# Optimization experiments

Measured on AMD Instinct MI355X. Metric: run time of the kernel, lower is better.

The kernel has to match this reference:

```python
import jax, jax.numpy as jnp
import numpy as np

GC = 128      # mem_dim
HEADS = 4     # gc / att_head_dim
HD = 32       # att_head_dim


def _dwconv(x, w, b, pad):
    # depthwise conv, NCHW, weight OIHW with I=1, groups=GC
    y = jax.lax.conv_general_dilated(
        x, w, window_strides=(1, 1),
        padding=((pad[0], pad[0]), (pad[1], pad[1])),
        feature_group_count=GC,
        dimension_numbers=('NCHW', 'OIHW', 'NCHW'))
    return y + b[None, :, None, None]


def setup_inputs() -> dict:
    key = jax.random.key(0)
    ks = jax.random.split(key, 5)
    x = jax.random.normal(ks[0], (32, 512, 56, 56), dtype=jnp.float32)
    w_dw1 = jax.random.normal(ks[1], (GC, 1, 3, 3), dtype=jnp.float32) * 0.1
    b_dw1 = jnp.zeros((GC,), jnp.float32)
    w_dw2 = jax.random.normal(ks[2], (GC, 1, 7, 7), dtype=jnp.float32) * 0.05
    b_dw2 = jnp.zeros((GC,), jnp.float32)
    w_qk = jax.random.normal(ks[3], (2 * GC, GC, 1, 1), dtype=jnp.float32) * (1.0 / np.sqrt(GC))
    b_qk = jnp.zeros((2 * GC,), jnp.float32)
    return {"x": x, "w_dw1": w_dw1, "b_dw1": b_dw1, "w_dw2": w_dw2,
            "b_dw2": b_dw2, "w_qk": w_qk, "b_qk": b_qk}


def reference(x, w_dw1, b_dw1, w_dw2, b_dw2, w_qk, b_qk):
    B, C, H, W = x.shape
    HW = H * W
    # grasp_memory + asymmetric_decouple (split along channels)
    m0 = C - 3 * GC
    mem = x[:, :m0]
    feat_att = x[:, m0:m0 + GC]
    feat_conv1 = x[:, m0 + GC:m0 + 2 * GC]
    feat_conv2 = x[:, m0 + 2 * GC:]
    feat_conv1 = _dwconv(feat_conv1, w_dw1, b_dw1, (1, 1))
    feat_conv2 = _dwconv(feat_conv2, w_dw2, b_dw2, (3, 3))
    # 1x1 conv qk -> [B, 2*GC, H, W]
    qk = jnp.einsum('bchw,oc->bohw', feat_att, w_qk[:, :, 0, 0]) + b_qk[None, :, None, None]
    qk = qk.reshape(B, 2 * GC, HW)
    q = qk[:, :GC].reshape(B, HEADS, HD, HW).transpose(0, 1, 3, 2)   # [B,h,HW,d]
    k = qk[:, GC:].reshape(B, HEADS, HD, HW).transpose(0, 1, 3, 2)
    v = feat_att.reshape(B, HEADS, HD, HW).transpose(0, 1, 3, 2)
    q = jax.nn.elu(q) + 1.0
    k = jax.nn.elu(k) + 1.0
    kmean = k.mean(axis=2, keepdims=True)                            # [B,h,1,d]
    z = 1.0 / (jnp.einsum('bhnd,bhmd->bhnm', q, kmean) + 1e-6)       # [B,h,HW,1]
    kv = jnp.einsum('bhnd,bhne->bhde', k, v) / HW                    # [B,h,d,d]
    att = jnp.einsum('bhnd,bhde->bhne', q, kv) * z                   # [B,h,HW,d]
    feat_att_out = att.transpose(0, 1, 3, 2).reshape(B, GC, H, W)
    feats = jnp.concatenate([feat_att_out, feat_conv1, feat_conv2], axis=1)
    return (mem, feats)
```

## Files before the change

kernel.cpp:

```cpp
#include <hip/hip_runtime.h>
#include <hip/hip_bf16.h>

#define Bn   32
#define Cn   512
#define GCn  128
#define HWn  3136
#define M0   128

#define Q_ELEMS  (Bn*GCn*HWn)
#define KV_ELEMS (Bn*4*32*32)
#define KS_ELEMS (Bn*4*32)

typedef __attribute__((ext_vector_type(8))) short bf16x8;
typedef __attribute__((ext_vector_type(4))) float f32x4;

__device__ __forceinline__ float bf2f(unsigned short u) {
    union { unsigned int i; float f; } v; v.i = ((unsigned int)u) << 16; return v.f;
}
__device__ __forceinline__ unsigned short f2bf(float f) {
    union { __hip_bfloat16 h; unsigned short u; } v; v.h = __float2bfloat16(f); return v.u;
}
__device__ __forceinline__ float act_elu1(float v) {
    return v > 0.0f ? v + 1.0f : __expf(v);
}

__global__ __launch_bounds__(256) void k_pre(
    const float* __restrict__ w_qk, unsigned short* __restrict__ wfrag,
    float* __restrict__ kvz) {
    const int t = threadIdx.x;
    if (blockIdx.x < 128) {
        int idx = blockIdx.x * 256 + t;
        int j  = idx & 7;
        int l  = (idx >> 3) & 63;
        int ks = (idx >> 9) & 3;
        int mt = idx >> 11;
        int o = mt * 16 + (l & 15);
        int c = ks * 32 + (l >> 4) * 8 + j;
        wfrag[idx] = f2bf(w_qk[o * 128 + c]);
    } else {
        int i = (blockIdx.x - 128) * 256 + t;
        kvz[i] = 0.0f;
    }
}

__global__ __launch_bounds__(256) void k_main(
    const float* __restrict__ x, const unsigned short* __restrict__ wfrag,
    const float* __restrict__ b_qk,
    unsigned short* __restrict__ q_ws, float* __restrict__ kv_g,
    float* __restrict__ ks_g) {

    __shared__ unsigned short Xn[64 * 144];
    __shared__ unsigned short Klds[128 * 72];
    unsigned short* Qlds = Xn;

    const int t  = threadIdx.x;
    const int n0 = blockIdx.x * 64;
    const int b  = blockIdx.y;
    const float* xa = x + ((long long)(b * Cn + M0)) * HWn;

    {
        const int c0 = t >> 1, half = t & 1;
        const float* src = xa + (long long)c0 * HWn + n0 + half * 32;
        #pragma unroll
        for (int p = 0; p < 8; ++p) {
            float4 v = *(const float4*)(src + p * 4);
            const int n = half * 32 + p * 4;
            Xn[(n + 0) * 144 + c0] = f2bf(v.x);
            Xn[(n + 1) * 144 + c0] = f2bf(v.y);
            Xn[(n + 2) * 144 + c0] = f2bf(v.z);
            Xn[(n + 3) * 144 + c0] = f2bf(v.w);
        }
    }
    __syncthreads();

    const int w = t >> 6, l = t & 63, nn = l & 15, q = l >> 4;
    f32x4 acc[4][4] = {};

    #pragma unroll
    for (int ks = 0; ks < 4; ++ks) {
        bf16x8 bq[4];
        #pragma unroll
        for (int in = 0; in < 4; ++in)
            bq[in] = *(const bf16x8*)(Xn + (in * 16 + nn) * 144 + ks * 32 + q * 8);
        #pragma unroll
        for (int im = 0; im < 4; ++im) {
            const int mt = 4 * w + im;
            bf16x8 aq = *(const bf16x8*)(wfrag + ((mt * 4 + ks) * 64 + l) * 8);
            #pragma unroll
            for (int in = 0; in < 4; ++in)
                acc[im][in] = __builtin_amdgcn_mfma_f32_16x16x32_bf16(aq, bq[in], acc[im][in], 0, 0, 0);
        }
    }

    if (w >= 2) {
        #pragma unroll
        for (int im = 0; im < 4; ++im) {
            const int obase = w * 64 + im * 16 + q * 4;
            float4 bias4 = *(const float4*)(b_qk + obase);
            const int krow = obase - 128;
            #pragma unroll
            for (int r = 0; r < 4; ++r) {
                const float bias = ((const float*)&bias4)[r];
                #pragma unroll
                for (int in = 0; in < 4; ++in)
                    Klds[(krow + r) * 72 + in * 16 + nn] = f2bf(act_elu1(acc[im][in][r] + bias));
            }
        }
    }
    __syncthreads();

    if (w < 2) {
        #pragma unroll
        for (int im = 0; im < 4; ++im) {
            const int obase = w * 64 + im * 16 + q * 4;
            float4 bias4 = *(const float4*)(b_qk + obase);
            #pragma unroll
            for (int r = 0; r < 4; ++r) {
                const float bias = ((const float*)&bias4)[r];
                #pragma unroll
                for (int in = 0; in < 4; ++in)
                    Qlds[(obase + r) * 72 + in * 16 + nn] = f2bf(act_elu1(acc[im][in][r] + bias));
            }
        }
    }

    {
        const int h = w;
        f32x4 akv[2][2] = {};
        float ksl0 = 0.0f, ksl1 = 0.0f;
        #pragma unroll
        for (int kt = 0; kt < 2; ++kt) {
            bf16x8 af0 = *(const bf16x8*)(Klds + (h * 32 + nn) * 72 + kt * 32 + q * 8);
            bf16x8 af1 = *(const bf16x8*)(Klds + (h * 32 + 16 + nn) * 72 + kt * 32 + q * 8);
            {
                const unsigned short* a0 = (const unsigned short*)&af0;
                const unsigned short* a1 = (const unsigned short*)&af1;
                #pragma unroll
                for (int j = 0; j < 8; ++j) { ksl0 += bf2f(a0[j]); ksl1 += bf2f(a1[j]); }
            }
            #pragma unroll
            for (int nt = 0; nt < 2; ++nt) {
                const float* vsrc = xa + (long long)(h * 32 + nt * 16 + nn) * HWn + n0 + kt * 32 + q * 8;
                float4 v0 = *(const float4*)(vsrc);
                float4 v1 = *(const float4*)(vsrc + 4);
                short tb[8];
                tb[0] = (short)f2bf(v0.x); tb[1] = (short)f2bf(v0.y);
                tb[2] = (short)f2bf(v0.z); tb[3] = (short)f2bf(v0.w);
                tb[4] = (short)f2bf(v1.x); tb[5] = (short)f2bf(v1.y);
                tb[6] = (short)f2bf(v1.z); tb[7] = (short)f2bf(v1.w);
                bf16x8 bv = *(bf16x8*)tb;
                akv[0][nt] = __builtin_amdgcn_mfma_f32_16x16x32_bf16(af0, bv, akv[0][nt], 0, 0, 0);
                akv[1][nt] = __builtin_amdgcn_mfma_f32_16x16x32_bf16(af1, bv, akv[1][nt], 0, 0, 0);
            }
        }
        const int bh = b * 4 + h;
        #pragma unroll
        for (int mt = 0; mt < 2; ++mt)
            #pragma unroll
            for (int nt = 0; nt < 2; ++nt)
                #pragma unroll
                for (int r = 0; r < 4; ++r)
                    atomicAdd(&kv_g[(bh << 10) + (mt * 16 + q * 4 + r) * 32 + nt * 16 + nn],
                              akv[mt][nt][r]);
        float s0 = ksl0; s0 += __shfl_xor(s0, 16, 64); s0 += __shfl_xor(s0, 32, 64);
        float s1 = ksl1; s1 += __shfl_xor(s1, 16, 64); s1 += __shfl_xor(s1, 32, 64);
        if (l < 16) {
            atomicAdd(&ks_g[bh * 32 + nn],      s0);
            atomicAdd(&ks_g[bh * 32 + 16 + nn], s1);
        }
    }
    __syncthreads();

    {
        const int row = t >> 1, hf = t & 1;
        const unsigned short* sp = Qlds + row * 72 + hf * 32;
        unsigned short* dp = q_ws + ((long long)(b * GCn + row)) * HWn + n0 + hf * 32;
        #pragma unroll
        for (int p = 0; p < 4; ++p)
            *(bf16x8*)(dp + p * 8) = *(const bf16x8*)(sp + p * 8);
    }
}

__device__ __forceinline__ void att_dev(
    const unsigned short* __restrict__ q_ws, const float* __restrict__ kv_g,
    const float* __restrict__ ks_g, float* __restrict__ feats,
    float* kvl, float* kml, int gx, int h, int b) {

    const int t = threadIdx.x;
    const int bh = b * 4 + h;
    const float inv = 1.0f / 3136.0f;
    #pragma unroll
    for (int p = 0; p < 4; ++p) kvl[t + p * 256] = kv_g[(bh << 10) + t + p * 256] * inv;
    if (t < 32) kml[t] = ks_g[bh * 32 + t] * inv;
    __syncthreads();

    const int n2 = gx * 256 + t;
    if (n2 >= 1568) return;
    const unsigned short* qp = q_ws + ((long long)(b * GCn + h * 32)) * HWn + n2 * 2;
    float a0[32], a1[32];
    float z0 = 1e-6f, z1 = 1e-6f;
    #pragma unroll
    for (int e = 0; e < 32; ++e) { a0[e] = 0.f; a1[e] = 0.f; }
    #pragma unroll 4
    for (int d = 0; d < 32; ++d) {
        const unsigned int qq = *(const unsigned int*)(qp + (long long)d * HWn);
        const float q0 = bf2f((unsigned short)qq);
        const float q1 = bf2f((unsigned short)(qq >> 16));
        z0 = __builtin_fmaf(q0, kml[d], z0);
        z1 = __builtin_fmaf(q1, kml[d], z1);
        #pragma unroll
        for (int e = 0; e < 32; ++e) {
            const float kv = kvl[d * 32 + e];
            a0[e] = __builtin_fmaf(q0, kv, a0[e]);
            a1[e] = __builtin_fmaf(q1, kv, a1[e]);
        }
    }
    z0 = 1.f / z0; z1 = 1.f / z1;
    float* op = feats + ((long long)(b * 384 + h * 32)) * HWn + n2 * 2;
    #pragma unroll
    for (int e = 0; e < 32; ++e)
        *(float2*)(op + (long long)e * HWn) = make_float2(a0[e] * z0, a1[e] * z1);
}

template<int KS, int PAD, int CIN, int COUT>
__device__ __forceinline__ void dwconv_dev(
    const float* __restrict__ x, const float* __restrict__ wg,
    const float* __restrict__ bg, float* __restrict__ feats,
    float* P, int c, int b) {

    const int t = threadIdx.x;
    const float* in = x + ((long long)(b * Cn + CIN + c)) * HWn;
    float* op = feats + ((long long)(b * 384 + COUT + c)) * HWn;

    constexpr int ROWS = 56 + 2 * PAD;
    const float4 z4 = make_float4(0.f, 0.f, 0.f, 0.f);
    for (int i = t; i < (ROWS * 68) >> 2; i += 256) ((float4*)P)[i] = z4;
    __syncthreads();
    for (int i = t; i < 784; i += 256) {
        const int y = i / 14, xq = (i % 14) * 4;
        *(float4*)(P + (y + PAD) * 68 + 4 + xq) = *(const float4*)(in + y * 56 + xq);
    }
    __syncthreads();

    float wr[KS * KS];
    #pragma unroll
    for (int i = 0; i < KS * KS; ++i) wr[i] = wg[c * KS * KS + i];
    const float bias = bg[c];

    for (int item = t; item < 392; item += 256) {
        const int y  = item / 7;
        const int xo = (item - y * 7) * 8;
        float acc[8];
        #pragma unroll
        for (int j = 0; j < 8; ++j) acc[j] = bias;
        #pragma unroll
        for (int dy = 0; dy < KS; ++dy) {
            const float* rp = P + (y + dy) * 68 + xo;
            float r[16];
            #pragma unroll
            for (int u = 0; u < 4; ++u) *(float4*)(r + 4 * u) = *(const float4*)(rp + 4 * u);
            #pragma unroll
            for (int dx = 0; dx < KS; ++dx) {
                const float wv = wr[dy * KS + dx];
                #pragma unroll
                for (int j = 0; j < 8; ++j)
                    acc[j] = __builtin_fmaf(wv, r[j + dx + 4 - PAD], acc[j]);
            }
        }
        *(float4*)(op + y * 56 + xo)     = make_float4(acc[0], acc[1], acc[2], acc[3]);
        *(float4*)(op + y * 56 + xo + 4) = make_float4(acc[4], acc[5], acc[6], acc[7]);
    }
}

__global__ __launch_bounds__(256) void k_post(
    const float* __restrict__ x,
    const unsigned short* __restrict__ q_ws, const float* __restrict__ kv_g,
    const float* __restrict__ ks_g,
    const float* __restrict__ w_dw1, const float* __restrict__ b_dw1,
    const float* __restrict__ w_dw2, const float* __restrict__ b_dw2,
    float* __restrict__ mem_out, float* __restrict__ feats) {

    __shared__ float smem[62 * 68];
    const int bid = blockIdx.x;

    if (bid < 4096) {
        dwconv_dev<7, 3, 384, 256>(x, w_dw2, b_dw2, feats, smem, bid & 127, bid >> 7);
    } else if (bid < 8192) {
        const int r = bid - 4096;
        dwconv_dev<3, 1, 256, 128>(x, w_dw1, b_dw1, feats, smem, r & 127, r >> 7);
    } else if (bid < 9088) {
        const int r = bid - 8192;
        const int b = r / 28, rem = r % 28;
        att_dev(q_ws, kv_g, ks_g, feats, smem, smem + 1024, rem % 7, rem / 7, b);
    } else {
        const int r = bid - 9088;
        for (int i4 = r * 256 + (int)threadIdx.x; i4 < 3211264; i4 += 2048 * 256) {
            int b  = i4 / 100352;
            int rr = i4 - b * 100352;
            ((float4*)mem_out)[i4] = ((const float4*)x)[(long long)b * 401408 + rr];
        }
    }
}

extern "C" void kernel_launch(void* const* d_in, const int* in_sizes, int n_in,
                              void* d_out, int out_size, void* d_ws, size_t ws_size,
                              hipStream_t stream) {
    const float* x     = (const float*)d_in[0];
    const float* w_dw1 = (const float*)d_in[1];
    const float* b_dw1 = (const float*)d_in[2];
    const float* w_dw2 = (const float*)d_in[3];
    const float* b_dw2 = (const float*)d_in[4];
    const float* w_qk  = (const float*)d_in[5];
    const float* b_qk  = (const float*)d_in[6];
    float* out = (float*)d_out;

    unsigned short* q_ws = (unsigned short*)d_ws;
    float* kv_g = (float*)(q_ws + (long long)Q_ELEMS);
    float* ks_g = kv_g + KV_ELEMS;
    unsigned short* wfrag = (unsigned short*)(ks_g + KS_ELEMS);

    float* mem_out = out;
    float* feats   = out + (long long)Bn * GCn * HWn;

    k_pre <<<656, 256, 0, stream>>>(w_qk, wfrag, kv_g);
    k_main<<<dim3(49, 32), 256, 0, stream>>>(x, wfrag, b_qk, q_ws, kv_g, ks_g);
    k_post<<<11136, 256, 0, stream>>>(x, q_ws, kv_g, ks_g,
                                      w_dw1, b_dw1, w_dw2, b_dw2, mem_out, feats);
}
```

Before: 451.3 us.

## Move mem copy into main kernel and process two channels, two rows per dwconv thread

The mem passthrough copy moves from the post kernel into the main qk/kv kernel, where its blocks run alongside the MFMA blocks to fill idle bandwidth. The depthwise conv now handles two channels per block, and each thread computes two output rows so that loaded LDS rows are reused across vertically adjacent outputs. The LDS tile uses an XOR-swizzled 64-float pitch to avoid bank conflicts. This raises register pressure and LDS size per block, and the fused kernel's mixed block types may contend for resources.

```diff
diff --git a/kernel.cpp b/kernel.cpp
--- a/kernel.cpp
+++ b/kernel.cpp
@@ -43,19 +43,17 @@
     }
 }
 
-__global__ __launch_bounds__(256) void k_main(
+__device__ __forceinline__ void main_dev(
     const float* __restrict__ x, const unsigned short* __restrict__ wfrag,
     const float* __restrict__ b_qk,
     unsigned short* __restrict__ q_ws, float* __restrict__ kv_g,
-    float* __restrict__ ks_g) {
-
-    __shared__ unsigned short Xn[64 * 144];
-    __shared__ unsigned short Klds[128 * 72];
+    float* __restrict__ ks_g,
+    unsigned short* Xn, unsigned short* Klds, int nt, int b) {
+
     unsigned short* Qlds = Xn;
 
     const int t  = threadIdx.x;
-    const int n0 = blockIdx.x * 64;
-    const int b  = blockIdx.y;
+    const int n0 = nt * 64;
     const float* xa = x + ((long long)(b * Cn + M0)) * HWn;
 
     {
@@ -139,8 +137,8 @@
                 for (int j = 0; j < 8; ++j) { ksl0 += bf2f(a0[j]); ksl1 += bf2f(a1[j]); }
             }
             #pragma unroll
-            for (int nt = 0; nt < 2; ++nt) {
-                const float* vsrc = xa + (long long)(h * 32 + nt * 16 + nn) * HWn + n0 + kt * 32 + q * 8;
+            for (int vt = 0; vt < 2; ++vt) {
+                const float* vsrc = xa + (long long)(h * 32 + vt * 16 + nn) * HWn + n0 + kt * 32 + q * 8;
                 float4 v0 = *(const float4*)(vsrc);
                 float4 v1 = *(const float4*)(vsrc + 4);
                 short tb[8];
@@ -149,19 +147,19 @@
                 tb[4] = (short)f2bf(v1.x); tb[5] = (short)f2bf(v1.y);
                 tb[6] = (short)f2bf(v1.z); tb[7] = (short)f2bf(v1.w);
                 bf16x8 bv = *(bf16x8*)tb;
-                akv[0][nt] = __builtin_amdgcn_mfma_f32_16x16x32_bf16(af0, bv, akv[0][nt], 0, 0, 0);
-                akv[1][nt] = __builtin_amdgcn_mfma_f32_16x16x32_bf16(af1, bv, akv[1][nt], 0, 0, 0);
+                akv[0][vt] = __builtin_amdgcn_mfma_f32_16x16x32_bf16(af0, bv, akv[0][vt], 0, 0, 0);
+                akv[1][vt] = __builtin_amdgcn_mfma_f32_16x16x32_bf16(af1, bv, akv[1][vt], 0, 0, 0);
             }
         }
         const int bh = b * 4 + h;
         #pragma unroll
         for (int mt = 0; mt < 2; ++mt)
             #pragma unroll
-            for (int nt = 0; nt < 2; ++nt)
+            for (int vt = 0; vt < 2; ++vt)
                 #pragma unroll
                 for (int r = 0; r < 4; ++r)
-                    atomicAdd(&kv_g[(bh << 10) + (mt * 16 + q * 4 + r) * 32 + nt * 16 + nn],
-                              akv[mt][nt][r]);
+                    atomicAdd(&kv_g[(bh << 10) + (mt * 16 + q * 4 + r) * 32 + vt * 16 + nn],
+                              akv[mt][vt][r]);
         float s0 = ksl0; s0 += __shfl_xor(s0, 16, 64); s0 += __shfl_xor(s0, 32, 64);
         float s1 = ksl1; s1 += __shfl_xor(s1, 16, 64); s1 += __shfl_xor(s1, 32, 64);
         if (l < 16) {
@@ -178,6 +176,28 @@
         #pragma unroll
         for (int p = 0; p < 4; ++p)
             *(bf16x8*)(dp + p * 8) = *(const bf16x8*)(sp + p * 8);
+    }
+}
+
+__global__ __launch_bounds__(256) void k_maincopy(
+    const float* __restrict__ x, const unsigned short* __restrict__ wfrag,
+    const float* __restrict__ b_qk,
+    unsigned short* __restrict__ q_ws, float* __restrict__ kv_g,
+    float* __restrict__ ks_g, float* __restrict__ mem_out) {
+
+    __shared__ __align__(16) unsigned char smem[36864];
+    const int bid = blockIdx.x;
+    if (bid < 1568) {
+        main_dev(x, wfrag, b_qk, q_ws, kv_g, ks_g,
+                 (unsigned short*)smem, (unsigned short*)(smem + 18432),
+                 bid % 49, bid / 49);
+    } else {
+        const int r = bid - 1568;
+        for (int i4 = r * 256 + (int)threadIdx.x; i4 < 3211264; i4 += 2048 * 256) {
+            int b  = i4 / 100352;
+            int rr = i4 - b * 100352;
+            ((float4*)mem_out)[i4] = ((const float4*)x)[(long long)b * 401408 + rr];
+        }
     }
 }
 
@@ -222,83 +242,101 @@
         *(float2*)(op + (long long)e * HWn) = make_float2(a0[e] * z0, a1[e] * z1);
 }
 
-template<int KS, int PAD, int CIN, int COUT>
-__device__ __forceinline__ void dwconv_dev(
+template<int KS, int PAD, int CIN>
+__device__ __forceinline__ void dwconv2_dev(
     const float* __restrict__ x, const float* __restrict__ wg,
     const float* __restrict__ bg, float* __restrict__ feats,
-    float* P, int c, int b) {
+    float* P, int cp, int b) {
 
     const int t = threadIdx.x;
-    const float* in = x + ((long long)(b * Cn + CIN + c)) * HWn;
-    float* op = feats + ((long long)(b * 384 + COUT + c)) * HWn;
-
     constexpr int ROWS = 56 + 2 * PAD;
+    constexpr int PL = ROWS * 64;
+    const int c0 = cp * 2;
+
     const float4 z4 = make_float4(0.f, 0.f, 0.f, 0.f);
-    for (int i = t; i < (ROWS * 68) >> 2; i += 256) ((float4*)P)[i] = z4;
-    __syncthreads();
-    for (int i = t; i < 784; i += 256) {
-        const int y = i / 14, xq = (i % 14) * 4;
-        *(float4*)(P + (y + PAD) * 68 + 4 + xq) = *(const float4*)(in + y * 56 + xq);
-    }
-    __syncthreads();
-
-    float wr[KS * KS];
-    #pragma unroll
-    for (int i = 0; i < KS * KS; ++i) wr[i] = wg[c * KS * KS + i];
-    const float bias = bg[c];
+    for (int i = t; i < (2 * PL) >> 2; i += 256) ((float4*)P)[i] = z4;
+    __syncthreads();
+
+    for (int i = t; i < 1568; i += 256) {
+        const int ch = (i >= 784) ? 1 : 0;
+        const int r  = i - ch * 784;
+        const int y  = r / 14, k = r - y * 14;
+        const float* in = x + ((long long)(b * Cn + CIN + c0 + ch)) * HWn + y * 56 + k * 4;
+        const int row = y + PAD;
+        const int ck  = (1 + k) ^ (row & 7);
+        *(float4*)(P + ch * PL + row * 64 + ck * 4) = *(const float4*)in;
+    }
+    __syncthreads();
 
     for (int item = t; item < 392; item += 256) {
-        const int y  = item / 7;
-        const int xo = (item - y * 7) * 8;
-        float acc[8];
-        #pragma unroll
-        for (int j = 0; j < 8; ++j) acc[j] = bias;
-        #pragma unroll
-        for (int dy = 0; dy < KS; ++dy) {
-            const float* rp = P + (y + dy) * 68 + xo;
-            float r[16];
-            #pragma unroll
-            for (int u = 0; u < 4; ++u) *(float4*)(r + 4 * u) = *(const float4*)(rp + 4 * u);
-            #pragma unroll
-            for (int dx = 0; dx < KS; ++dx) {
-                const float wv = wr[dy * KS + dx];
-                #pragma unroll
-                for (int j = 0; j < 8; ++j)
-                    acc[j] = __builtin_fmaf(wv, r[j + dx + 4 - PAD], acc[j]);
-            }
-        }
-        *(float4*)(op + y * 56 + xo)     = make_float4(acc[0], acc[1], acc[2], acc[3]);
-        *(float4*)(op + y * 56 + xo + 4) = make_float4(acc[4], acc[5], acc[6], acc[7]);
-    }
-}
-
-__global__ __launch_bounds__(256) void k_post(
+        const int ch = (item >= 196) ? 1 : 0;
+        const int r  = item - ch * 196;
+        const int ri = r / 7, m = r - ri * 7;
+        const int y0 = ri * 2;
+        const int xo = m * 8;
+        const float* wp = wg + (c0 + ch) * KS * KS;
+        const float bias = bg[c0 + ch];
+        const float* Pc = P + ch * PL;
+        float* op = feats + ((long long)(b * 384 + (CIN - 128) + c0 + ch)) * HWn;
+
+        float a0[8], a1[8];
+        #pragma unroll
+        for (int j = 0; j < 8; ++j) { a0[j] = bias; a1[j] = bias; }
+        #pragma unroll
+        for (int dy = 0; dy <= KS; ++dy) {
+            const int row = y0 + dy;
+            float rr[16];
+            #pragma unroll
+            for (int u = 0; u < 4; ++u) {
+                const int ck = ((xo >> 2) + u) ^ (row & 7);
+                *(float4*)(rr + 4 * u) = *(const float4*)(Pc + row * 64 + ck * 4);
+            }
+            if (dy < KS) {
+                #pragma unroll
+                for (int dx = 0; dx < KS; ++dx) {
+                    const float wv = wp[dy * KS + dx];
+                    #pragma unroll
+                    for (int j = 0; j < 8; ++j)
+                        a0[j] = __builtin_fmaf(wv, rr[j + dx + 4 - PAD], a0[j]);
+                }
+            }
+            if (dy >= 1) {
+                #pragma unroll
+                for (int dx = 0; dx < KS; ++dx) {
+                    const float wv = wp[(dy - 1) * KS + dx];
+                    #pragma unroll
+                    for (int j = 0; j < 8; ++j)
+                        a1[j] = __builtin_fmaf(wv, rr[j + dx + 4 - PAD], a1[j]);
+                }
+            }
+        }
+        *(float4*)(op + y0 * 56 + xo)           = make_float4(a0[0], a0[1], a0[2], a0[3]);
+        *(float4*)(op + y0 * 56 + xo + 4)       = make_float4(a0[4], a0[5], a0[6], a0[7]);
+        *(float4*)(op + (y0 + 1) * 56 + xo)     = make_float4(a1[0], a1[1], a1[2], a1[3]);
+        *(float4*)(op + (y0 + 1) * 56 + xo + 4) = make_float4(a1[4], a1[5], a1[6], a1[7]);
+    }
+}
+
+__global__ __launch_bounds__(256) void k_post2(
     const float* __restrict__ x,
     const unsigned short* __restrict__ q_ws, const float* __restrict__ kv_g,
     const float* __restrict__ ks_g,
     const float* __restrict__ w_dw1, const float* __restrict__ b_dw1,
     const float* __restrict__ w_dw2, const float* __restrict__ b_dw2,
-    float* __restrict__ mem_out, float* __restrict__ feats) {
-
-    __shared__ float smem[62 * 68];
+    float* __restrict__ feats) {
+
+    __shared__ __align__(16) float smem[2 * 62 * 64];
     const int bid = blockIdx.x;
 
-    if (bid < 4096) {
-        dwconv_dev<7, 3, 384, 256>(x, w_dw2, b_dw2, feats, smem, bid & 127, bid >> 7);
-    } else if (bid < 8192) {
+    if (bid < 2048) {
+        dwconv2_dev<7, 3, 384>(x, w_dw2, b_dw2, feats, smem, bid & 63, bid >> 6);
+    } else if (bid < 4096) {
+        const int r = bid - 2048;
+        dwconv2_dev<3, 1, 256>(x, w_dw1, b_dw1, feats, smem, r & 63, r >> 6);
+    } else {
         const int r = bid - 4096;
-        dwconv_dev<3, 1, 256, 128>(x, w_dw1, b_dw1, feats, smem, r & 127, r >> 7);
-    } else if (bid < 9088) {
-        const int r = bid - 8192;
         const int b = r / 28, rem = r % 28;
         att_dev(q_ws, kv_g, ks_g, feats, smem, smem + 1024, rem % 7, rem / 7, b);
-    } else {
-        const int r = bid - 9088;
-        for (int i4 = r * 256 + (int)threadIdx.x; i4 < 3211264; i4 += 2048 * 256) {
-            int b  = i4 / 100352;
-            int rr = i4 - b * 100352;
-            ((float4*)mem_out)[i4] = ((const float4*)x)[(long long)b * 401408 + rr];
-        }
     }
 }
 
@@ -322,8 +360,8 @@
     float* mem_out = out;
     float* feats   = out + (long long)Bn * GCn * HWn;
 
-    k_pre <<<656, 256, 0, stream>>>(w_qk, wfrag, kv_g);
-    k_main<<<dim3(49, 32), 256, 0, stream>>>(x, wfrag, b_qk, q_ws, kv_g, ks_g);
-    k_post<<<11136, 256, 0, stream>>>(x, q_ws, kv_g, ks_g,
-                                      w_dw1, b_dw1, w_dw2, b_dw2, mem_out, feats);
-}
+    k_pre     <<<656, 256, 0, stream>>>(w_qk, wfrag, kv_g);
+    k_maincopy<<<3616, 256, 0, stream>>>(x, wfrag, b_qk, q_ws, kv_g, ks_g, mem_out);
+    k_post2   <<<4992, 256, 0, stream>>>(x, q_ws, kv_g, ks_g,
+                                         w_dw1, b_dw1, w_dw2, b_dw2, feats);
+}
```

New measurement: 439.7 us. -2.6%, faster.
